# Kernel optimization log

Measured on AMD Instinct MI355X. Metric: run time of the kernel, lower is better.

Reference implementation:

```python
import jax, jax.numpy as jnp
import numpy as np

B, S, D = 8, 4096, 1024
G, V = 2, 320
TAU = 1.0
EPS = 1e-7


def setup_inputs() -> dict:
    key = jax.random.key(0)
    k_x, k_w, k_cb, k_u = jax.random.split(key, 4)
    x = jax.random.normal(k_x, (B, S, D), dtype=jnp.float32)
    W = jax.random.normal(k_w, (D, G * V), dtype=jnp.float32) * (1.0 / np.sqrt(D))
    b = jnp.zeros((G * V,), dtype=jnp.float32)
    # nn.init.uniform_ -> U(0,1); codebooks viewed as [G, V, D//G]
    codebooks = jax.random.uniform(k_cb, (G, V, D // G), dtype=jnp.float32)
    # standard Gumbel(0,1) noise, one per logit: shape [B*S*G, V]
    u = jax.random.uniform(k_u, (B * S * G, V), dtype=jnp.float32,
                           minval=1e-6, maxval=1.0 - 1e-6)
    gumbel = -jnp.log(-jnp.log(u))
    return {"x": x, "W": W, "b": b, "codebooks": codebooks, "gumbel": gumbel}


def reference(x, W, b, codebooks, gumbel):
    Bx, Sx, Dx = x.shape
    Gx, Vx, _ = codebooks.shape
    N = Bx * Sx
    # logit projection: [B,S,D] @ [D, G*V] -> flatten to [N*G, V]
    logits = (jnp.einsum('bsd,de->bse', x, W) + b).reshape(N * Gx, Vx)
    # gumbel-softmax, hard=True with straight-through estimator
    y_soft = jax.nn.softmax((logits + gumbel) / TAU, axis=-1)
    idx = jnp.argmax(y_soft, axis=-1)
    y_hard = jax.nn.one_hot(idx, Vx, dtype=y_soft.dtype)
    one_hot_st = y_hard + y_soft - jax.lax.stop_gradient(y_soft)  # fwd == y_hard
    # codebook lookup via (mostly one-hot) contraction: [N,G,V] x [G,V,d] -> [N,G,d]
    q = jnp.einsum('ngv,gvd->ngd', one_hot_st.reshape(N, Gx, Vx), codebooks)
    quantized = q.reshape(Bx, Sx, Dx)
    # perplexity from clean (non-gumbel) softmax probs
    probs = jax.nn.softmax(logits.reshape(N, Gx, Vx), axis=-1)
    avg_probs = probs.mean(axis=0)  # [G, V]
    perplexity = jnp.exp(-jnp.sum(avg_probs * jnp.log(avg_probs + EPS), axis=-1)).mean()
    return (quantized, perplexity)
```

## Files before the change

### kernel.cpp

```cpp
#include <hip/hip_runtime.h>
#include <hip/hip_bf16.h>
#include <math.h>

#define NROWS 32768
#define DD    1024
#define EE    640
#define VV    320
#define BM    128
#define KT    32
#define CTN   40

typedef __attribute__((ext_vector_type(8))) short short8;
typedef __attribute__((ext_vector_type(4))) short short4v;
typedef __attribute__((ext_vector_type(4))) float float4v;

static __device__ __forceinline__ unsigned short f2bf(float f) {
    unsigned int u = __float_as_uint(f);
    return (unsigned short)((u + 0x7fffu + ((u >> 16) & 1u)) >> 16);
}

static __device__ __forceinline__ void gload_lds16(const void* g, void* l) {
    __builtin_amdgcn_global_load_lds(
        (const __attribute__((address_space(1))) unsigned int*)g,
        (__attribute__((address_space(3))) unsigned int*)l, 16, 0, 0);
}

__global__ void pack_w(const float* __restrict__ W, unsigned short* __restrict__ bp)
{
    const int t = threadIdx.x;
    const int tile = blockIdx.x * 4 + (t >> 6);
    const int lane = t & 63;
    const int kt = tile / CTN, ct = tile % CTN;
    const int k0 = kt * 32 + (lane >> 4) * 8;
    const int col = ct * 16 + (lane & 15);
    unsigned short v1[8];
    #pragma unroll
    for (int e = 0; e < 8; ++e)
        v1[e] = f2bf(W[(size_t)(k0 + e) * EE + col]);
    *(short8*)(bp + ((size_t)tile * 64 + lane) * 8) = *(const short8*)v1;
}

__global__ __launch_bounds__(1024, 4) void fused_mfma(
    const float* __restrict__ x, const unsigned short* __restrict__ bp,
    const float* __restrict__ bias, const float* __restrict__ cb,
    const float* __restrict__ gum, float* __restrict__ out,
    float* __restrict__ probs_acc)
{
    __shared__ unsigned short Bs[3][32 * EE];
    __shared__ unsigned short As[2][BM * 32];
    __shared__ float probs_blk[EE];
    __shared__ float pmax[8][BM];
    __shared__ float psum[8][BM];
    __shared__ int   pidx[8][BM];
    __shared__ int   fidx[BM][2];
    __shared__ float finv[BM][2];

    const int t    = threadIdx.x;
    const int lane = t & 63;
    const int w    = t >> 6;
    const int rg   = w >> 3;
    const int cg   = w & 7;
    const int n0   = blockIdx.x * BM;

    float4v acc[4][5];
    #pragma unroll
    for (int rf = 0; rf < 4; ++rf)
        #pragma unroll
        for (int ct = 0; ct < 5; ++ct)
            acc[rf][ct] = (float4v)0.f;

    const int r0 = t >> 3, kq0 = t & 7;
    const int abase = (r0 >> 4)*512 + ((r0 & 15) + ((kq0 >> 1) << 4))*8 + ((kq0 & 1) << 2);
    const float* xr = x + (size_t)(n0 + r0) * DD + kq0 * 4;

    auto writeA = [&](int bb, float4 v) {
        short4v s1;
        s1[0] = (short)f2bf(v.x); s1[1] = (short)f2bf(v.y);
        s1[2] = (short)f2bf(v.z); s1[3] = (short)f2bf(v.w);
        *(short4v*)&As[bb][abase] = s1;
    };
    const int q0 = t, q1 = t + 1024, q2 = (t < 512) ? t + 2048 : t + 1536;
    auto stageB = [&](int bb, int kt) {
        const unsigned short* src = bp + (size_t)kt * (32 * EE);
        gload_lds16(src + (size_t)q0 * 8, &Bs[bb][q0 * 8]);
        gload_lds16(src + (size_t)q1 * 8, &Bs[bb][q1 * 8]);
        gload_lds16(src + (size_t)q2 * 8, &Bs[bb][q2 * 8]);
    };

    auto kbody = [&](int i, int b0, int bstg, float4& curA, float4& nxtA) {
        asm volatile("s_waitcnt vmcnt(4) lgkmcnt(0)" ::: "memory");
        __builtin_amdgcn_s_barrier();
        __builtin_amdgcn_sched_barrier(0);
        if (i + 2 < KT) {
            stageB(bstg, i + 2);
            nxtA = *(const float4*)(xr + (size_t)(i + 2) * 32);
        }
        __builtin_amdgcn_sched_barrier(0);
        short8 af[4];
        #pragma unroll
        for (int rf = 0; rf < 4; ++rf)
            af[rf] = *(const short8*)&As[i & 1][(rg*4 + rf)*512 + lane*8];
        #pragma unroll
        for (int ct = 0; ct < 5; ++ct) {
            short8 bf = *(const short8*)&Bs[b0][((cg*5 + ct)*64 + lane)*8];
            #pragma unroll
            for (int rf = 0; rf < 4; ++rf)
                acc[rf][ct] = __builtin_amdgcn_mfma_f32_16x16x32_bf16(af[rf], bf, acc[rf][ct], 0, 0, 0);
        }
        __builtin_amdgcn_sched_barrier(0);
        if (i + 1 < KT) writeA((i + 1) & 1, curA);
    };

    float4 pA0, pA1;
    {
        stageB(0, 0);
        float4 a00 = *(const float4*)(xr);
        stageB(1, 1);
        pA0 = *(const float4*)(xr + 32);
        __builtin_amdgcn_sched_barrier(0);
        writeA(0, a00);
    }

    int bc = 0;
    for (int i = 0; i < KT; i += 2) {
        const int b1 = (bc + 1 > 2) ? 0 : bc + 1;
        const int b2 = (bc + 2 > 2) ? bc - 1 : bc + 2;
        kbody(i,     bc, b2, pA0, pA1);
        kbody(i + 1, b1, bc, pA1, pA0);
        bc = b2;
    }

    {
        float bv[5];
        #pragma unroll
        for (int ct = 0; ct < 5; ++ct) bv[ct] = bias[cg*80 + ct*16 + (lane & 15)];
        #pragma unroll
        for (int rf = 0; rf < 4; ++rf)
            #pragma unroll
            for (int ct = 0; ct < 5; ++ct) {
                acc[rf][ct][0] += bv[ct]; acc[rf][ct][1] += bv[ct];
                acc[rf][ct][2] += bv[ct]; acc[rf][ct][3] += bv[ct];
            }
    }

    const int g = cg >> 2;
    const int goff0 = (cg & 3)*80 + (lane & 15);
    #pragma unroll
    for (int rf = 0; rf < 4; ++rf) {
        #pragma unroll
        for (int r = 0; r < 4; ++r) {
            const int rowA = rg*64 + rf*16 + ((lane >> 4) << 2) + r;
            const float* grow = gum + ((size_t)(n0 + rowA)*2 + g)*VV + goff0;
            float m1 = -1e30f; int bi = 0; float es = 0.f;
            #pragma unroll
            for (int ct = 0; ct < 5; ++ct) {
                float z  = acc[rf][ct][r];
                float zg = z + grow[ct*16];
                if (zg > m1) { m1 = zg; bi = goff0 + ct*16; }
                es += __expf(z);
            }
            #pragma unroll
            for (int off = 1; off < 16; off <<= 1) {
                float om = __shfl_xor(m1, off);
                int   ob = __shfl_xor(bi, off);
                if (om > m1 || (om == m1 && ob < bi)) { m1 = om; bi = ob; }
                es += __shfl_xor(es, off);
            }
            if ((lane & 15) == 0) {
                pmax[cg][rowA] = m1; pidx[cg][rowA] = bi; psum[cg][rowA] = es;
            }
        }
    }
    for (int c = t; c < EE; c += 1024) probs_blk[c] = 0.f;
    __syncthreads();

    if (t < 256) {
        const int row = t & 127, gg = t >> 7;
        float m1 = -1e30f; int bi = 0x7fffffff; float s = 0.f;
        #pragma unroll
        for (int c = 0; c < 4; ++c) {
            const float om = pmax[gg*4 + c][row];
            const int   ob = pidx[gg*4 + c][row];
            if (om > m1 || (om == m1 && ob < bi)) { m1 = om; bi = ob; }
            s += psum[gg*4 + c][row];
        }
        fidx[row][gg] = bi;
        finv[row][gg] = 1.f / s;
    }
    __syncthreads();

    float pacc[5];
    #pragma unroll
    for (int ct = 0; ct < 5; ++ct) pacc[ct] = 0.f;
    #pragma unroll
    for (int rf = 0; rf < 4; ++rf) {
        #pragma unroll
        for (int r = 0; r < 4; ++r) {
            const int rowA = rg*64 + rf*16 + ((lane >> 4) << 2) + r;
            const float inv = finv[rowA][g];
            #pragma unroll
            for (int ct = 0; ct < 5; ++ct)
                pacc[ct] += __expf(acc[rf][ct][r]) * inv;
        }
    }
    #pragma unroll
    for (int off = 16; off < 64; off <<= 1)
        #pragma unroll
        for (int ct = 0; ct < 5; ++ct)
            pacc[ct] += __shfl_xor(pacc[ct], off);
    if (lane < 16) {
        #pragma unroll
        for (int ct = 0; ct < 5; ++ct)
            atomicAdd(&probs_blk[cg*80 + ct*16 + lane], pacc[ct]);
    }
    __syncthreads();

    for (int c = t; c < EE; c += 1024)
        atomicAdd(&probs_acc[c], probs_blk[c]);

    for (int i = t; i < BM*256; i += 1024) {
        const int row = i >> 8, f4 = i & 255;
        const int gg  = f4 >> 7;
        const int idx = fidx[row][gg];
        const float4 v = *(const float4*)&cb[((size_t)gg*VV + idx)*512 + (size_t)(f4 & 127)*4];
        *(float4*)&out[(size_t)(n0 + row)*DD + (size_t)f4*4] = v;
    }
}

__global__ void perp_kernel(const float* __restrict__ probs_acc,
                            float* __restrict__ outp)
{
    __shared__ float s0[4], s1[4];
    int t = threadIdx.x;
    float p0 = 0.f, p1 = 0.f;
    for (int c = t; c < EE; c += 256) {
        float a = probs_acc[c] * (1.0f / NROWS);
        float v = a * logf(a + 1e-7f);
        if (c < VV) p0 += v; else p1 += v;
    }
    #pragma unroll
    for (int off = 1; off < 64; off <<= 1) {
        p0 += __shfl_xor(p0, off);
        p1 += __shfl_xor(p1, off);
    }
    if ((t & 63) == 0) { s0[t >> 6] = p0; s1[t >> 6] = p1; }
    __syncthreads();
    if (t == 0) {
        float a0 = s0[0] + s0[1] + s0[2] + s0[3];
        float a1 = s1[0] + s1[1] + s1[2] + s1[3];
        outp[0] = 0.5f * (expf(-a0) + expf(-a1));
    }
}

extern "C" void kernel_launch(void* const* d_in, const int* in_sizes, int n_in,
                              void* d_out, int out_size, void* d_ws, size_t ws_size,
                              hipStream_t stream)
{
    const float* x   = (const float*)d_in[0];
    const float* W   = (const float*)d_in[1];
    const float* b   = (const float*)d_in[2];
    const float* cb  = (const float*)d_in[3];
    const float* gum = (const float*)d_in[4];
    float* out = (float*)d_out;

    unsigned short* bp = (unsigned short*)d_ws;
    float* probs_acc = (float*)((char*)d_ws + (size_t)DD*EE*2);

    hipMemsetAsync(probs_acc, 0, EE * sizeof(float), stream);
    pack_w<<<320, 256, 0, stream>>>(W, bp);
    fused_mfma<<<NROWS / BM, 1024, 0, stream>>>(x, bp, b, cb, gum, out, probs_acc);
    perp_kernel<<<1, 256, 0, stream>>>(probs_acc, out + (out_size - 1));
}
```

Measured before the change: 128.8 us.

## Split codebook gather out of fused GEMM kernel and merge perplexity into it

After: 128.6 us. About the same (-0.1%).

```diff
diff --git a/kernel.cpp b/kernel.cpp
--- a/kernel.cpp
+++ b/kernel.cpp
@@ -40,11 +40,10 @@
     *(short8*)(bp + ((size_t)tile * 64 + lane) * 8) = *(const short8*)v1;
 }
 
-__global__ __launch_bounds__(1024, 4) void fused_mfma(
+__global__ __launch_bounds__(1024, 4) void logits_kernel(
     const float* __restrict__ x, const unsigned short* __restrict__ bp,
-    const float* __restrict__ bias, const float* __restrict__ cb,
-    const float* __restrict__ gum, float* __restrict__ out,
-    float* __restrict__ probs_acc)
+    const float* __restrict__ bias, const float* __restrict__ gum,
+    int* __restrict__ gfidx, float* __restrict__ probs_acc)
 {
     __shared__ unsigned short Bs[3][32 * EE];
     __shared__ unsigned short As[2][BM * 32];
@@ -52,7 +51,6 @@
     __shared__ float pmax[8][BM];
     __shared__ float psum[8][BM];
     __shared__ int   pidx[8][BM];
-    __shared__ int   fidx[BM][2];
     __shared__ float finv[BM][2];
 
     const int t    = threadIdx.x;
@@ -184,7 +182,7 @@
             if (om > m1 || (om == m1 && ob < bi)) { m1 = om; bi = ob; }
             s += psum[gg*4 + c][row];
         }
-        fidx[row][gg] = bi;
+        gfidx[(size_t)(n0 + row)*2 + gg] = bi;
         finv[row][gg] = 1.f / s;
     }
     __syncthreads();
@@ -217,38 +215,45 @@
 
     for (int c = t; c < EE; c += 1024)
         atomicAdd(&probs_acc[c], probs_blk[c]);
-
-    for (int i = t; i < BM*256; i += 1024) {
-        const int row = i >> 8, f4 = i & 255;
-        const int gg  = f4 >> 7;
-        const int idx = fidx[row][gg];
-        const float4 v = *(const float4*)&cb[((size_t)gg*VV + idx)*512 + (size_t)(f4 & 127)*4];
-        *(float4*)&out[(size_t)(n0 + row)*DD + (size_t)f4*4] = v;
-    }
-}
-
-__global__ void perp_kernel(const float* __restrict__ probs_acc,
-                            float* __restrict__ outp)
-{
+}
+
+__global__ __launch_bounds__(256) void gather_kernel(
+    const float* __restrict__ cb, const int* __restrict__ gfidx,
+    const float* __restrict__ probs_acc, float* __restrict__ out, int out_size)
+{
+    __shared__ int sidx[8][2];
     __shared__ float s0[4], s1[4];
-    int t = threadIdx.x;
-    float p0 = 0.f, p1 = 0.f;
-    for (int c = t; c < EE; c += 256) {
-        float a = probs_acc[c] * (1.0f / NROWS);
-        float v = a * logf(a + 1e-7f);
-        if (c < VV) p0 += v; else p1 += v;
-    }
-    #pragma unroll
-    for (int off = 1; off < 64; off <<= 1) {
-        p0 += __shfl_xor(p0, off);
-        p1 += __shfl_xor(p1, off);
-    }
-    if ((t & 63) == 0) { s0[t >> 6] = p0; s1[t >> 6] = p1; }
-    __syncthreads();
-    if (t == 0) {
-        float a0 = s0[0] + s0[1] + s0[2] + s0[3];
-        float a1 = s1[0] + s1[1] + s1[2] + s1[3];
-        outp[0] = 0.5f * (expf(-a0) + expf(-a1));
+    const int t  = threadIdx.x;
+    const int r0 = blockIdx.x * 8;
+    if (t < 16) sidx[t >> 1][t & 1] = gfidx[(size_t)(r0 + (t >> 1)) * 2 + (t & 1)];
+    __syncthreads();
+    const int gg = t >> 7;
+    const int f4 = t & 127;
+    #pragma unroll
+    for (int r = 0; r < 8; ++r) {
+        const int idx = sidx[r][gg];
+        const float4 v = *(const float4*)&cb[((size_t)gg*VV + idx)*512 + (size_t)f4*4];
+        *(float4*)&out[(size_t)(r0 + r)*DD + (size_t)t*4] = v;
+    }
+    if (blockIdx.x == 0) {
+        float p0 = 0.f, p1 = 0.f;
+        for (int c = t; c < EE; c += 256) {
+            float a = probs_acc[c] * (1.0f / NROWS);
+            float v = a * logf(a + 1e-7f);
+            if (c < VV) p0 += v; else p1 += v;
+        }
+        #pragma unroll
+        for (int off = 1; off < 64; off <<= 1) {
+            p0 += __shfl_xor(p0, off);
+            p1 += __shfl_xor(p1, off);
+        }
+        if ((t & 63) == 0) { s0[t >> 6] = p0; s1[t >> 6] = p1; }
+        __syncthreads();
+        if (t == 0) {
+            float a0 = s0[0] + s0[1] + s0[2] + s0[3];
+            float a1 = s1[0] + s1[1] + s1[2] + s1[3];
+            out[out_size - 1] = 0.5f * (expf(-a0) + expf(-a1));
+        }
     }
 }
 
@@ -265,9 +270,10 @@
 
     unsigned short* bp = (unsigned short*)d_ws;
     float* probs_acc = (float*)((char*)d_ws + (size_t)DD*EE*2);
+    int*   gfidx     = (int*)((char*)d_ws + (size_t)DD*EE*2 + 4096);
 
     hipMemsetAsync(probs_acc, 0, EE * sizeof(float), stream);
     pack_w<<<320, 256, 0, stream>>>(W, bp);
-    fused_mfma<<<NROWS / BM, 1024, 0, stream>>>(x, bp, b, cb, gum, out, probs_acc);
-    perp_kernel<<<1, 256, 0, stream>>>(probs_acc, out + (out_size - 1));
-}
+    logits_kernel<<<NROWS / BM, 1024, 0, stream>>>(x, bp, b, gum, gfidx, probs_acc);
+    gather_kernel<<<NROWS / 8, 256, 0, stream>>>(cb, gfidx, probs_acc, out, out_size);
+}
```

## Split B staging into parity half-tiles with six-slot ring and replicated prob atomics

Applied to the files above, without the earlier changes.

After: 322.5 us. +150.5%, slower.

```diff
diff --git a/kernel.cpp b/kernel.cpp
--- a/kernel.cpp
+++ b/kernel.cpp
@@ -18,7 +18,6 @@
     unsigned int u = __float_as_uint(f);
     return (unsigned short)((u + 0x7fffu + ((u >> 16) & 1u)) >> 16);
 }
-
 static __device__ __forceinline__ void gload_lds16(const void* g, void* l) {
     __builtin_amdgcn_global_load_lds(
         (const __attribute__((address_space(1))) unsigned int*)g,
@@ -40,13 +39,13 @@
     *(short8*)(bp + ((size_t)tile * 64 + lane) * 8) = *(const short8*)v1;
 }
 
-__global__ __launch_bounds__(1024, 4) void fused_mfma(
+__global__ __launch_bounds__(1024, 4) void fused_vq(
     const float* __restrict__ x, const unsigned short* __restrict__ bp,
     const float* __restrict__ bias, const float* __restrict__ cb,
     const float* __restrict__ gum, float* __restrict__ out,
-    float* __restrict__ probs_acc)
+    float* __restrict__ probs_rep)
 {
-    __shared__ unsigned short Bs[3][32 * EE];
+    __shared__ unsigned short Bs[6][20 * 512];
     __shared__ unsigned short As[2][BM * 32];
     __shared__ float probs_blk[EE];
     __shared__ float pmax[8][BM];
@@ -62,12 +61,41 @@
     const int cg   = w & 7;
     const int n0   = blockIdx.x * BM;
 
+    int g1e = 0, g2e = 0, g1o = 0, g2o = 0;
+    {
+        int cnt0 = 0, cnt1 = 0;
+        #pragma unroll
+        for (int c = 0; c < 8; ++c)
+            #pragma unroll
+            for (int j = 0; j < 5; ++j) {
+                const int f = c * 5 + j;
+                if (((j + c) & 1) == 0) {
+                    if (cnt0 == w) g1e = f;
+                    if (cnt0 == 16 + (w & 3)) g2e = f;
+                    ++cnt0;
+                } else {
+                    if (cnt1 == w) g1o = f;
+                    if (cnt1 == 16 + (w & 3)) g2o = f;
+                    ++cnt1;
+                }
+            }
+    }
+    const int b0 = (cg >> 1) * 5 + (cg & 1) * 3;
+    const int b1 = (cg >> 1) * 5 + (cg & 1) * 2;
+    int jpar[5], jidx[5];
+    #pragma unroll
+    for (int j = 0; j < 5; ++j) {
+        jpar[j] = (j + cg) & 1;
+        jidx[j] = (jpar[j] ? b1 : b0) + (j >> 1);
+    }
+
     float4v acc[4][5];
     #pragma unroll
     for (int rf = 0; rf < 4; ++rf)
         #pragma unroll
         for (int ct = 0; ct < 5; ++ct)
             acc[rf][ct] = (float4v)0.f;
+    short8 af[4];
 
     const int r0 = t >> 3, kq0 = t & 7;
     const int abase = (r0 >> 4)*512 + ((r0 & 15) + ((kq0 >> 1) << 4))*8 + ((kq0 & 1) << 2);
@@ -79,56 +107,106 @@
         s1[2] = (short)f2bf(v.z); s1[3] = (short)f2bf(v.w);
         *(short4v*)&As[bb][abase] = s1;
     };
-    const int q0 = t, q1 = t + 1024, q2 = (t < 512) ? t + 2048 : t + 1536;
-    auto stageB = [&](int bb, int kt) {
-        const unsigned short* src = bp + (size_t)kt * (32 * EE);
-        gload_lds16(src + (size_t)q0 * 8, &Bs[bb][q0 * 8]);
-        gload_lds16(src + (size_t)q1 * 8, &Bs[bb][q1 * 8]);
-        gload_lds16(src + (size_t)q2 * 8, &Bs[bb][q2 * 8]);
-    };
-
-    auto kbody = [&](int i, int b0, int bstg, float4& curA, float4& nxtA) {
-        asm volatile("s_waitcnt vmcnt(4) lgkmcnt(0)" ::: "memory");
+    auto ldA = [&](int ab) {
+        #pragma unroll
+        for (int rf = 0; rf < 4; ++rf)
+            af[rf] = *(const short8*)&As[ab][(rg*4 + rf)*512 + lane*8];
+    };
+    auto stg = [&](int slotS, int ktS, int ga, int gb, bool dup) {
+        const unsigned short* src = bp + (size_t)ktS * (CTN * 512);
+        unsigned short* db = &Bs[slotS][0];
+        gload_lds16(src + ((size_t)ga*64 + lane)*8, db + ((size_t)(w*64 + lane))*8);
+        gload_lds16(src + ((size_t)gb*64 + lane)*8, db + ((size_t)((16 + (w & 3))*64 + lane))*8);
+        if (dup)
+            gload_lds16(src + ((size_t)ga*64 + lane)*8, db + ((size_t)(w*64 + lane))*8);
+    };
+    auto mm = [&](int slotU, int parv) {
+        #pragma unroll
+        for (int j = 0; j < 5; ++j) {
+            if (jpar[j] == parv) {
+                short8 bf = *(const short8*)&Bs[slotU][(size_t)jidx[j]*512 + lane*8];
+                #pragma unroll
+                for (int rf = 0; rf < 4; ++rf)
+                    acc[rf][j] = __builtin_amdgcn_mfma_f32_16x16x32_bf16(af[rf], bf, acc[rf][j], 0, 0, 0);
+            }
+        }
+    };
+
+    float4 pXa, pXb;
+    {
+        float4 a00 = *(const float4*)(xr);
+        pXb = *(const float4*)(xr + 32);
+        stg(0, 0, g1e, g2e, true);
+        stg(1, 0, g1o, g2o, true);
+        stg(2, 1, g1e, g2e, true);
+        stg(3, 1, g1o, g2o, true);
+        __builtin_amdgcn_sched_barrier(0);
+        writeA(0, a00);
+        asm volatile("s_waitcnt lgkmcnt(0)" ::: "memory");
         __builtin_amdgcn_s_barrier();
-        __builtin_amdgcn_sched_barrier(0);
-        if (i + 2 < KT) {
-            stageB(bstg, i + 2);
-            nxtA = *(const float4*)(xr + (size_t)(i + 2) * 32);
-        }
-        __builtin_amdgcn_sched_barrier(0);
-        short8 af[4];
-        #pragma unroll
-        for (int rf = 0; rf < 4; ++rf)
-            af[rf] = *(const short8*)&As[i & 1][(rg*4 + rf)*512 + lane*8];
-        #pragma unroll
-        for (int ct = 0; ct < 5; ++ct) {
-            short8 bf = *(const short8*)&Bs[b0][((cg*5 + ct)*64 + lane)*8];
-            #pragma unroll
-            for (int rf = 0; rf < 4; ++rf)
-                acc[rf][ct] = __builtin_amdgcn_mfma_f32_16x16x32_bf16(af[rf], bf, acc[rf][ct], 0, 0, 0);
-        }
-        __builtin_amdgcn_sched_barrier(0);
-        if (i + 1 < KT) writeA((i + 1) & 1, curA);
-    };
-
-    float4 pA0, pA1;
-    {
-        stageB(0, 0);
-        float4 a00 = *(const float4*)(xr);
-        stageB(1, 1);
-        pA0 = *(const float4*)(xr + 32);
-        __builtin_amdgcn_sched_barrier(0);
-        writeA(0, a00);
-    }
-
-    int bc = 0;
-    for (int i = 0; i < KT; i += 2) {
-        const int b1 = (bc + 1 > 2) ? 0 : bc + 1;
-        const int b2 = (bc + 2 > 2) ? bc - 1 : bc + 2;
-        kbody(i,     bc, b2, pA0, pA1);
-        kbody(i + 1, b1, bc, pA1, pA0);
-        bc = b2;
-    }
+    }
+
+    auto ktbody = [&](int kt, float4& LR, float4& UR,
+                      int su, int s1, int s4, int s5) {
+        asm volatile("s_waitcnt vmcnt(9) lgkmcnt(0)" ::: "memory");
+        __builtin_amdgcn_s_barrier();
+        __builtin_amdgcn_sched_barrier(0);
+        stg(s4, kt + 2, g1e, g2e, false);
+        LR = *(const float4*)(xr + (size_t)(kt + 2) * 32);
+        __builtin_amdgcn_sched_barrier(0);
+        ldA(kt & 1);
+        __builtin_amdgcn_s_setprio(1);
+        mm(su, 0);
+        __builtin_amdgcn_s_setprio(0);
+        __builtin_amdgcn_sched_barrier(0);
+        asm volatile("s_waitcnt vmcnt(9) lgkmcnt(0)" ::: "memory");
+        __builtin_amdgcn_s_barrier();
+        __builtin_amdgcn_sched_barrier(0);
+        stg(s5, kt + 2, g1o, g2o, true);
+        __builtin_amdgcn_sched_barrier(0);
+        __builtin_amdgcn_s_setprio(1);
+        mm(s1, 1);
+        __builtin_amdgcn_s_setprio(0);
+        __builtin_amdgcn_sched_barrier(0);
+        writeA((kt + 1) & 1, UR);
+    };
+
+    int su = 0;
+    for (int kt = 0; kt < KT - 2; kt += 2) {
+        int s1 = su + 1; if (s1 >= 6) s1 -= 6;
+        int s4 = su + 4; if (s4 >= 6) s4 -= 6;
+        int s5 = su + 5; if (s5 >= 6) s5 -= 6;
+        ktbody(kt, pXa, pXb, su, s1, s4, s5);
+        su += 2; if (su >= 6) su -= 6;
+        s1 = su + 1; if (s1 >= 6) s1 -= 6;
+        s4 = su + 4; if (s4 >= 6) s4 -= 6;
+        s5 = su + 5; if (s5 >= 6) s5 -= 6;
+        ktbody(kt + 1, pXb, pXa, su, s1, s4, s5);
+        su += 2; if (su >= 6) su -= 6;
+    }
+    asm volatile("s_waitcnt vmcnt(0) lgkmcnt(0)" ::: "memory");
+    __builtin_amdgcn_s_barrier();
+    __builtin_amdgcn_sched_barrier(0);
+    ldA((KT - 2) & 1);
+    __builtin_amdgcn_s_setprio(1); mm(0, 0); __builtin_amdgcn_s_setprio(0);
+    __builtin_amdgcn_sched_barrier(0);
+    asm volatile("s_waitcnt lgkmcnt(0)" ::: "memory");
+    __builtin_amdgcn_s_barrier();
+    __builtin_amdgcn_sched_barrier(0);
+    __builtin_amdgcn_s_setprio(1); mm(1, 1); __builtin_amdgcn_s_setprio(0);
+    __builtin_amdgcn_sched_barrier(0);
+    writeA((KT - 1) & 1, pXb);
+    asm volatile("s_waitcnt lgkmcnt(0)" ::: "memory");
+    __builtin_amdgcn_s_barrier();
+    __builtin_amdgcn_sched_barrier(0);
+    ldA((KT - 1) & 1);
+    __builtin_amdgcn_s_setprio(1); mm(2, 0); __builtin_amdgcn_s_setprio(0);
+    __builtin_amdgcn_sched_barrier(0);
+    asm volatile("s_waitcnt lgkmcnt(0)" ::: "memory");
+    __builtin_amdgcn_s_barrier();
+    __builtin_amdgcn_sched_barrier(0);
+    __builtin_amdgcn_s_setprio(1); mm(3, 1); __builtin_amdgcn_s_setprio(0);
+    __builtin_amdgcn_sched_barrier(0);
 
     {
         float bv[5];
@@ -154,10 +232,10 @@
             float m1 = -1e30f; int bi = 0; float es = 0.f;
             #pragma unroll
             for (int ct = 0; ct < 5; ++ct) {
-                float z  = acc[rf][ct][r];
-                float zg = z + grow[ct*16];
+                float zv = acc[rf][ct][r];
+                float zg = zv + grow[ct*16];
                 if (zg > m1) { m1 = zg; bi = goff0 + ct*16; }
-                es += __expf(z);
+                es += __expf(zv);
             }
             #pragma unroll
             for (int off = 1; off < 16; off <<= 1) {
@@ -215,8 +293,9 @@
     }
     __syncthreads();
 
+    const int rep = blockIdx.x & 7;
     for (int c = t; c < EE; c += 1024)
-        atomicAdd(&probs_acc[c], probs_blk[c]);
+        atomicAdd(&probs_rep[rep*EE + c], probs_blk[c]);
 
     for (int i = t; i < BM*256; i += 1024) {
         const int row = i >> 8, f4 = i & 255;
@@ -227,14 +306,17 @@
     }
 }
 
-__global__ void perp_kernel(const float* __restrict__ probs_acc,
-                            float* __restrict__ outp)
+__global__ void perp8_kernel(const float* __restrict__ probs_rep,
+                             float* __restrict__ outp)
 {
     __shared__ float s0[4], s1[4];
     int t = threadIdx.x;
     float p0 = 0.f, p1 = 0.f;
     for (int c = t; c < EE; c += 256) {
-        float a = probs_acc[c] * (1.0f / NROWS);
+        float a = 0.f;
+        #pragma unroll
+        for (int rp = 0; rp < 8; ++rp) a += probs_rep[rp*EE + c];
+        a *= (1.0f / NROWS);
         float v = a * logf(a + 1e-7f);
         if (c < VV) p0 += v; else p1 += v;
     }
@@ -263,11 +345,14 @@
     const float* gum = (const float*)d_in[4];
     float* out = (float*)d_out;
 
-    unsigned short* bp = (unsigned short*)d_ws;
-    float* probs_acc = (float*)((char*)d_ws + (size_t)DD*EE*2);
-
-    hipMemsetAsync(probs_acc, 0, EE * sizeof(float), stream);
+    char* wsp = (char*)d_ws;
+    unsigned short* bp = (unsigned short*)wsp;
+    const size_t bp_b = (size_t)DD*EE*2;
+    float* probs_rep = (float*)(wsp + bp_b);
+    const size_t pr_b = 8*EE*sizeof(float);
+
+    hipMemsetAsync(probs_rep, 0, pr_b, stream);
     pack_w<<<320, 256, 0, stream>>>(W, bp);
-    fused_mfma<<<NROWS / BM, 1024, 0, stream>>>(x, bp, b, cb, gum, out, probs_acc);
-    perp_kernel<<<1, 256, 0, stream>>>(probs_acc, out + (out_size - 1));
-}
+    fused_vq<<<NROWS / BM, 1024, 0, stream>>>(x, bp, b, cb, gum, out, probs_rep);
+    perp8_kernel<<<1, 256, 0, stream>>>(probs_rep, out + (out_size - 1));
+}
```
